# Kernel tuning notes

Measured on AMD Instinct MI355X. Metric: run time of the kernel, lower is better.

The kernel has to match this reference:

```python
import jax, jax.numpy as jnp
import numpy as np

DIM = 1024
HEADS = 16
HEAD_DIM = DIM // HEADS
K = 13              # kernel_size (odd)
NS = K // 2         # neighborhood radius
SCALE = HEAD_DIM ** -0.5


def setup_inputs() -> dict:
    key = jax.random.key(0)
    ks = jax.random.split(key, 5)
    B, L = 2, 4096
    x = jax.random.normal(ks[0], (B, L, DIM), jnp.float32)
    qkv_w = jax.random.normal(ks[1], (3 * DIM, DIM), jnp.float32) * 0.02
    qkv_b = jnp.zeros((3 * DIM,), jnp.float32)
    rpb = jax.random.normal(ks[2], (HEADS, 2 * K - 1), jnp.float32) * 0.02  # trunc_normal std=0.02
    proj_w = jax.random.normal(ks[3], (DIM, DIM), jnp.float32) * 0.02
    proj_b = jnp.zeros((DIM,), jnp.float32)
    return dict(x=x, qkv_w=qkv_w, qkv_b=qkv_b, rpb=rpb, proj_w=proj_w, proj_b=proj_b)


def reference(x, qkv_w, qkv_b, rpb, proj_w, proj_b):
    B, L, C = x.shape
    # qkv projection (torch Linear convention: y = x @ W^T + b)
    qkv = (x @ qkv_w.T + qkv_b).reshape(B, L, 3, HEADS, HEAD_DIM).transpose(2, 0, 3, 1, 4)
    q, k, v = qkv[0] * SCALE, qkv[1], qkv[2]  # each [B, H, L, D]

    i = jnp.arange(L)
    # NATTEN 1D window start (dilation=1): clamp window fully inside [0, L)
    ni = jnp.clip(i - NS, 0, L - K)                       # [L]
    # relative-position-bias start index per query (NATTEN get_pb_start)
    pi = NS + jnp.where(i < NS, NS - i, 0) + jnp.where(i + NS >= L, L - i - 1 - NS, 0)  # [L]
    j = jnp.arange(K)
    nbr = ni[:, None] + j[None, :]                        # [L, K] neighbor key indices
    bidx = pi[:, None] + j[None, :]                       # [L, K] rpb indices in [0, 2K-2]

    kg = k[:, :, nbr, :]                                  # [B, H, L, K, D]
    vg = v[:, :, nbr, :]                                  # [B, H, L, K, D]

    attn = jnp.einsum('bhld,bhlkd->bhlk', q, kg) + rpb[:, bidx][None]  # [B, H, L, K]
    attn = jax.nn.softmax(attn, axis=-1)
    out = jnp.einsum('bhlk,bhlkd->bhld', attn, vg)        # [B, H, L, D]
    out = out.transpose(0, 2, 1, 3).reshape(B, L, C)
    return out @ proj_w.T + proj_b
```

## Files before the change

kernel.cpp:

```cpp
#include <hip/hip_runtime.h>
#include <hip/hip_bf16.h>

#define DIMC 1024
#define HEADS 16
#define HEAD_DIM 64
#define KWIN 13
#define NSH 6
#define LSEQ 4096
#define BATCH 2
#define NROWS (BATCH*LSEQ)
#define QKV_N (3*DIMC)
#define SCALE_Q 0.125f

#define TBLK 256
#define WROWS 268

typedef __attribute__((ext_vector_type(4))) float f32x4;
typedef __attribute__((ext_vector_type(8))) short bf16x8;

__device__ __forceinline__ void gload_lds16(const void* g, void* l) {
  __builtin_amdgcn_global_load_lds(
      (const __attribute__((address_space(1))) void*)g,
      (__attribute__((address_space(3))) void*)l, 16, 0, 0);
}

__device__ __forceinline__ void cvt8(uint4 r, float* f) {
  unsigned u[4] = {r.x, r.y, r.z, r.w};
#pragma unroll
  for (int w = 0; w < 4; w++) {
    f[2*w]   = __uint_as_float(u[w] << 16);
    f[2*w+1] = __uint_as_float(u[w] & 0xffff0000u);
  }
}

__global__ __launch_bounds__(256) void cast_kernel(const float* __restrict__ in,
                                                   __hip_bfloat16* __restrict__ out,
                                                   int n4) {
  int i = blockIdx.x * 256 + threadIdx.x;
  if (i >= n4) return;
  float4 v = ((const float4*)in)[i];
  union { short4 s; __hip_bfloat16 h[4]; } u;
  u.h[0] = __float2bfloat16(v.x);
  u.h[1] = __float2bfloat16(v.y);
  u.h[2] = __float2bfloat16(v.z);
  u.h[3] = __float2bfloat16(v.w);
  ((short4*)out)[i] = u.s;
}

template<int OUT_BF16>
__global__ __launch_bounds__(256) void gemm_bt(const __hip_bfloat16* __restrict__ A,
                                               const __hip_bfloat16* __restrict__ B,
                                               const float* __restrict__ bias,
                                               void* __restrict__ Cout,
                                               int M, int N, int K) {
  __shared__ __align__(16) __hip_bfloat16 As[128 * 32];
  __shared__ __align__(16) __hip_bfloat16 Bs[128 * 32];

  const int tid  = threadIdx.x;
  const int lane = tid & 63;
  const int wave = tid >> 6;
  const int m0 = blockIdx.y * 128;
  const int n0 = blockIdx.x * 128;
  const int wr = wave >> 1;
  const int wc = wave & 1;

  f32x4 acc[4][4] = {};

  const int rA0  = wave * 32 + (lane >> 2);
  const int kcol = (lane & 3) * 8;
  const __hip_bfloat16* gA = A + (size_t)(m0 + rA0) * K + kcol;
  const __hip_bfloat16* gB = B + (size_t)(n0 + rA0) * K + kcol;
  __hip_bfloat16* lA0 = As + wave * 1024;
  __hip_bfloat16* lA1 = As + wave * 1024 + 512;
  __hip_bfloat16* lB0 = Bs + wave * 1024;
  __hip_bfloat16* lB1 = Bs + wave * 1024 + 512;

  const int fr = lane & 15;
  const int fk = (lane >> 4) * 8;

  for (int k0 = 0; k0 < K; k0 += 32) {
    gload_lds16(gA,                  lA0);
    gload_lds16(gA + (size_t)16 * K, lA1);
    gload_lds16(gB,                  lB0);
    gload_lds16(gB + (size_t)16 * K, lB1);
    gA += 32;
    gB += 32;
    __syncthreads();

    bf16x8 af[4], bfr[4];
#pragma unroll
    for (int i = 0; i < 4; i++)
      af[i] = *(const bf16x8*)&As[(wr * 64 + i * 16 + fr) * 32 + fk];
#pragma unroll
    for (int i = 0; i < 4; i++)
      bfr[i] = *(const bf16x8*)&Bs[(wc * 64 + i * 16 + fr) * 32 + fk];

#pragma unroll
    for (int mi = 0; mi < 4; mi++)
#pragma unroll
      for (int ni = 0; ni < 4; ni++)
        acc[mi][ni] = __builtin_amdgcn_mfma_f32_16x16x32_bf16(af[mi], bfr[ni], acc[mi][ni], 0, 0, 0);

    __syncthreads();
  }

#pragma unroll
  for (int ni = 0; ni < 4; ni++) {
    const int col = n0 + wc * 64 + ni * 16 + (lane & 15);
    const float bv = bias[col];
#pragma unroll
    for (int mi = 0; mi < 4; mi++) {
      const int row = m0 + wr * 64 + mi * 16 + ((lane >> 4) << 2);
#pragma unroll
      for (int i = 0; i < 4; i++) {
        const float v = acc[mi][ni][i] + bv;
        if (OUT_BF16)
          ((__hip_bfloat16*)Cout)[(size_t)(row + i) * N + col] = __float2bfloat16(v);
        else
          ((float*)Cout)[(size_t)(row + i) * N + col] = v;
      }
    }
  }
}

__global__ __launch_bounds__(256, 2) void natten(const __hip_bfloat16* __restrict__ qkv,
                                                 const float* __restrict__ rpb,
                                                 __hip_bfloat16* __restrict__ att) {
  __shared__ __align__(16) unsigned char smem[2 * WROWS * 128];

  const int tid = threadIdx.x;
  const int tb  = blockIdx.x;
  const int h   = blockIdx.y;
  const int b   = blockIdx.z;
  const int t0  = tb * TBLK;

  int r0 = t0 - NSH;
  if (r0 < 0) r0 = 0;
  if (r0 > LSEQ - WROWS) r0 = LSEQ - WROWS;

  const __hip_bfloat16* kg = qkv + ((size_t)b * LSEQ + r0) * QKV_N + DIMC + h * HEAD_DIM;
  const __hip_bfloat16* vg = kg + DIMC;
#pragma unroll 1
  for (int i = tid; i < WROWS * 8; i += 256) {
    const int row = i >> 3, c = i & 7;
    const uint4 kk = *(const uint4*)(kg + (size_t)row * QKV_N + c * 8);
    const uint4 vv = *(const uint4*)(vg + (size_t)row * QKV_N + c * 8);
    const int off = row * 128 + ((c * 16) ^ ((row & 7) << 4));
    *(uint4*)(smem + off) = kk;
    *(uint4*)(smem + WROWS * 128 + off) = vv;
  }
  __syncthreads();

  const int t = t0 + tid;
  int ni = t - NSH;
  ni = ni < 0 ? 0 : (ni > LSEQ - KWIN ? LSEQ - KWIN : ni);
  const int rbase = ni - r0;
  const int pi = NSH + (t < NSH ? NSH - t : 0) + (t + NSH >= LSEQ ? LSEQ - t - 1 - NSH : 0);
  const float* rp = rpb + h * (2 * KWIN - 1) + pi;

  const __hip_bfloat16* qg = qkv + ((size_t)b * LSEQ + t) * QKV_N + h * HEAD_DIM;
  float qf[64];
#pragma unroll
  for (int c = 0; c < 8; c++) {
    uint4 qq = *(const uint4*)(qg + c * 8);
    cvt8(qq, qf + c * 8);
  }

  float p[KWIN];
#pragma unroll
  for (int j = 0; j < KWIN; j++) {
    const int row = rbase + j;
    const int sw = (row & 7) << 4;
    float s = 0.f;
#pragma unroll
    for (int c = 0; c < 8; c++) {
      uint4 kk = *(const uint4*)(smem + row * 128 + ((c * 16) ^ sw));
      float kf[8];
      cvt8(kk, kf);
#pragma unroll
      for (int e = 0; e < 8; e++) s += qf[c * 8 + e] * kf[e];
    }
    p[j] = s * SCALE_Q + rp[j];
  }

  float m = p[0];
#pragma unroll
  for (int j = 1; j < KWIN; j++) m = fmaxf(m, p[j]);
  float sum = 0.f;
#pragma unroll
  for (int j = 0; j < KWIN; j++) { p[j] = __expf(p[j] - m); sum += p[j]; }
  const float inv = 1.f / sum;
#pragma unroll
  for (int j = 0; j < KWIN; j++) p[j] *= inv;

  __hip_bfloat16* og = att + ((size_t)b * LSEQ + t) * DIMC + h * HEAD_DIM;
#pragma unroll
  for (int c = 0; c < 8; c++) {
    float acc[8] = {0.f, 0.f, 0.f, 0.f, 0.f, 0.f, 0.f, 0.f};
#pragma unroll
    for (int j = 0; j < KWIN; j++) {
      const int row = rbase + j;
      uint4 vv = *(const uint4*)(smem + WROWS * 128 + row * 128 + ((c * 16) ^ ((row & 7) << 4)));
      float vf[8];
      cvt8(vv, vf);
#pragma unroll
      for (int e = 0; e < 8; e++) acc[e] += p[j] * vf[e];
    }
    union { ushort us[8]; uint4 v; } o;
#pragma unroll
    for (int e = 0; e < 8; e++) {
      __hip_bfloat16 hb = __float2bfloat16(acc[e]);
      o.us[e] = *(ushort*)&hb;
    }
    *(uint4*)(og + c * 8) = o.v;
  }
}

extern "C" void kernel_launch(void* const* d_in, const int* in_sizes, int n_in,
                              void* d_out, int out_size, void* d_ws, size_t ws_size,
                              hipStream_t stream) {
  const float* x      = (const float*)d_in[0];
  const float* qkv_w  = (const float*)d_in[1];
  const float* qkv_b  = (const float*)d_in[2];
  const float* rpb    = (const float*)d_in[3];
  const float* proj_w = (const float*)d_in[4];
  const float* proj_b = (const float*)d_in[5];
  float* out = (float*)d_out;

  char* ws = (char*)d_ws;
  __hip_bfloat16* xb    = (__hip_bfloat16*)(ws);
  __hip_bfloat16* wqkv  = (__hip_bfloat16*)(ws + 16777216);
  __hip_bfloat16* wproj = (__hip_bfloat16*)(ws + 23068672);
  __hip_bfloat16* qkv   = (__hip_bfloat16*)(ws + 25165824);
  __hip_bfloat16* att   = (__hip_bfloat16*)(ws + 75497472);

  cast_kernel<<<(NROWS * DIMC / 4 + 255) / 256, 256, 0, stream>>>(x, xb, NROWS * DIMC / 4);
  cast_kernel<<<(QKV_N * DIMC / 4 + 255) / 256, 256, 0, stream>>>(qkv_w, wqkv, QKV_N * DIMC / 4);
  cast_kernel<<<(DIMC * DIMC / 4 + 255) / 256, 256, 0, stream>>>(proj_w, wproj, DIMC * DIMC / 4);

  gemm_bt<1><<<dim3(QKV_N / 128, NROWS / 128), 256, 0, stream>>>(
      xb, wqkv, qkv_b, (void*)qkv, NROWS, QKV_N, DIMC);

  natten<<<dim3(LSEQ / TBLK, HEADS, BATCH), 256, 0, stream>>>(qkv, rpb, att);

  gemm_bt<0><<<dim3(DIMC / 128, NROWS / 128), 256, 0, stream>>>(
      att, wproj, proj_b, (void*)out, NROWS, DIMC, DIMC);
}
```

Baseline: 149.5 us.

## Replace QKV GEMM with 256x256 tiled, double-buffered 8-wave pipelined kernel

Adds a new bf16 GEMM for the QKV projection with 256x256 tiles, 8 waves, 64-wide K steps, and double-buffered LDS fed by direct global-to-LDS loads. Fine-grained vmcnt waits, barriers and s_setprio interleave the staging with MFMA phases. Block IDs are remapped across XCDs, and the epilogue goes through LDS to write 16-byte bf16 stores. It aims to raise MFMA utilization and hide load latency in the largest GEMM, at the cost of 128KB of LDS and hand-scheduled code that is harder to keep correct. The loop runs NT/2 iterations, which assumes an even tile count; that holds for K=1024.

Measured after the change: 203.3 us. 1.36x slower.

```diff
diff --git a/kernel.cpp b/kernel.cpp
--- a/kernel.cpp
+++ b/kernel.cpp
@@ -47,6 +47,146 @@
   ((short4*)out)[i] = u.s;
 }
 
+#define PH_MID do { __builtin_amdgcn_s_barrier(); \
+  asm volatile("s_waitcnt lgkmcnt(0)" ::: "memory"); \
+  __builtin_amdgcn_sched_barrier(0); \
+  __builtin_amdgcn_s_setprio(1); } while (0)
+#define PH_END do { __builtin_amdgcn_s_setprio(0); \
+  __builtin_amdgcn_s_barrier(); } while (0)
+#define VMW4 do { asm volatile("s_waitcnt vmcnt(4)" ::: "memory"); \
+  __builtin_amdgcn_sched_barrier(0); } while (0)
+
+#define STG(gptr, ldsoff) do { \
+  gload_lds16((const void*)(gptr),      (void*)(smem + (ldsoff) + w * 2048)); \
+  gload_lds16((const void*)((gptr)+q8), (void*)(smem + (ldsoff) + w * 2048 + 1024)); \
+} while (0)
+#define STAGE_A(buf, h, t) STG(((h) ? gA1 : gA0) + (size_t)(t) * 64, (buf)*32768 + (h)*16384)
+#define STAGE_B(buf, h, t) STG(((h) ? gB1 : gB0) + (size_t)(t) * 64, 65536 + (buf)*32768 + (h)*16384)
+
+#define LD_A4(buf, mb) do { _Pragma("unroll") for (int mm = 0; mm < 4; mm++) { \
+    const char* p_ = smem + (buf)*32768 + (rA + ((mb) + mm) * 16) * 128; \
+    afr[mm][0] = *(const bf16x8*)(p_ + ck0); \
+    afr[mm][1] = *(const bf16x8*)(p_ + ck1); } } while (0)
+#define LD_B2(buf, nb, dst) do { _Pragma("unroll") for (int nn = 0; nn < 2; nn++) { \
+    const char* p_ = smem + 65536 + (buf)*32768 + (rB + ((nb) + nn) * 16) * 128; \
+    dst[nn][0] = *(const bf16x8*)(p_ + ck0); \
+    dst[nn][1] = *(const bf16x8*)(p_ + ck1); } } while (0)
+#define MM16(mb, bsel, bf) do { _Pragma("unroll") for (int mm = 0; mm < 4; mm++) \
+  _Pragma("unroll") for (int nn = 0; nn < 2; nn++) { \
+    acc[(mb)+mm][(bsel)*2+nn] = __builtin_amdgcn_mfma_f32_16x16x32_bf16(afr[mm][0], bf[nn][0], acc[(mb)+mm][(bsel)*2+nn], 0, 0, 0); \
+    acc[(mb)+mm][(bsel)*2+nn] = __builtin_amdgcn_mfma_f32_16x16x32_bf16(afr[mm][1], bf[nn][1], acc[(mb)+mm][(bsel)*2+nn], 0, 0, 0); } } while (0)
+
+__global__ __launch_bounds__(512, 2) void gemm8(const __hip_bfloat16* __restrict__ A,
+                                                const __hip_bfloat16* __restrict__ B,
+                                                const float* __restrict__ bias,
+                                                __hip_bfloat16* __restrict__ C,
+                                                int M, int N, int K) {
+  __shared__ __align__(16) char smem[131072];
+  const int tid  = threadIdx.x;
+  const int lane = tid & 63;
+  const int w    = tid >> 6;
+  const int wm   = w >> 2;
+  const int wn   = w & 3;
+  const int fr   = lane & 15;
+  const int fq   = (lane >> 4) & 3;
+
+  int id = blockIdx.x;
+  {
+    const int nwg = gridDim.x;
+    const int qq = nwg >> 3, rr = nwg & 7;
+    const int xcd = id & 7, off = id >> 3;
+    id = (xcd < rr ? xcd * (qq + 1) : rr * (qq + 1) + (xcd - rr) * qq) + off;
+  }
+  const int nbx = N >> 8;
+  const int bx = id % nbx, by = id / nbx;
+  const int m0 = by << 8, n0 = bx << 8;
+
+  const int srow = w * 16 + (lane >> 3);
+  const int gch  = ((lane & 7) ^ (lane >> 3)) * 8;
+  const __hip_bfloat16* gA0 = A + (size_t)(m0 + srow) * K + gch;
+  const __hip_bfloat16* gA1 = A + (size_t)(m0 + 128 + srow) * K + gch;
+  const __hip_bfloat16* gB0 = B + (size_t)(n0 + srow) * K + gch;
+  const __hip_bfloat16* gB1 = B + (size_t)(n0 + 128 + srow) * K + gch;
+  const size_t q8 = (size_t)8 * K;
+
+  const int rA  = wm * 128 + fr;
+  const int rB  = wn * 64 + fr;
+  const int ck0 = ((fq)     ^ (fr & 7)) * 16;
+  const int ck1 = ((4 | fq) ^ (fr & 7)) * 16;
+
+  f32x4 acc[8][4] = {};
+  bf16x8 afr[4][2], bfr0[2][2], bfr1[2][2];
+
+  STAGE_A(0, 0, 0); STAGE_A(0, 1, 0);
+  STAGE_B(0, 0, 0); STAGE_B(0, 1, 0);
+  STAGE_B(1, 0, 1); STAGE_B(1, 1, 1);
+  VMW4;
+  __builtin_amdgcn_s_barrier();
+
+  const int NT = K >> 6;
+  const int NI = NT >> 1;
+#pragma unroll 1
+  for (int i = 0; i < NI; i++) {
+    const int t1 = (2*i+1 < NT) ? 2*i+1 : NT-1;
+    const int t2 = (2*i+2 < NT) ? 2*i+2 : NT-1;
+    const int t3 = (2*i+3 < NT) ? 2*i+3 : NT-1;
+    LD_A4(0, 0); LD_B2(0, 0, bfr0);
+    STAGE_A(1, 0, t1);
+    PH_MID; MM16(0, 0, bfr0); PH_END;
+    LD_B2(0, 2, bfr1);
+    STAGE_A(1, 1, t1);
+    PH_MID; MM16(0, 1, bfr1); PH_END;
+    LD_A4(0, 4);
+    STAGE_B(0, 0, t2);
+    PH_MID; MM16(4, 0, bfr0); PH_END;
+    STAGE_B(0, 1, t2);
+    VMW4;
+    PH_MID; MM16(4, 1, bfr1); PH_END;
+    LD_A4(1, 0); LD_B2(1, 0, bfr0);
+    STAGE_A(0, 0, t2);
+    PH_MID; MM16(0, 0, bfr0); PH_END;
+    LD_B2(1, 2, bfr1);
+    STAGE_A(0, 1, t2);
+    PH_MID; MM16(0, 1, bfr1); PH_END;
+    LD_A4(1, 4);
+    STAGE_B(1, 0, t3);
+    PH_MID; MM16(4, 0, bfr0); PH_END;
+    STAGE_B(1, 1, t3);
+    VMW4;
+    PH_MID; MM16(4, 1, bfr1); PH_END;
+  }
+
+  asm volatile("s_waitcnt vmcnt(0)" ::: "memory");
+  __builtin_amdgcn_sched_barrier(0);
+  __builtin_amdgcn_s_barrier();
+
+  float* sf = (float*)(smem) + w * 1088;
+  float bv[4];
+#pragma unroll
+  for (int n = 0; n < 4; n++) bv[n] = bias[n0 + wn * 64 + n * 16 + fr];
+
+#pragma unroll 1
+  for (int m = 0; m < 8; m++) {
+#pragma unroll
+    for (int n = 0; n < 4; n++)
+#pragma unroll
+      for (int i = 0; i < 4; i++)
+        sf[(fq * 4 + i) * 68 + n * 16 + fr] = acc[m][n][i] + bv[n];
+    float v[16];
+#pragma unroll
+    for (int e = 0; e < 16; e++) v[e] = sf[fr * 68 + fq * 16 + e];
+    union { ushort us[16]; uint4 u4[2]; } o;
+#pragma unroll
+    for (int e = 0; e < 16; e++) {
+      __hip_bfloat16 hb = __float2bfloat16(v[e]);
+      o.us[e] = *(ushort*)&hb;
+    }
+    __hip_bfloat16* cp = C + (size_t)(m0 + wm * 128 + m * 16 + fr) * N + n0 + wn * 64 + fq * 16;
+    *(uint4*)(cp)     = o.u4[0];
+    *(uint4*)(cp + 8) = o.u4[1];
+  }
+}
+
 template<int OUT_BF16>
 __global__ __launch_bounds__(256) void gemm_bt(const __hip_bfloat16* __restrict__ A,
                                                const __hip_bfloat16* __restrict__ B,
@@ -238,8 +378,8 @@
   cast_kernel<<<(QKV_N * DIMC / 4 + 255) / 256, 256, 0, stream>>>(qkv_w, wqkv, QKV_N * DIMC / 4);
   cast_kernel<<<(DIMC * DIMC / 4 + 255) / 256, 256, 0, stream>>>(proj_w, wproj, DIMC * DIMC / 4);
 
-  gemm_bt<1><<<dim3(QKV_N / 128, NROWS / 128), 256, 0, stream>>>(
-      xb, wqkv, qkv_b, (void*)qkv, NROWS, QKV_N, DIMC);
+  gemm8<<<(NROWS / 256) * (QKV_N / 256), 512, 0, stream>>>(
+      xb, wqkv, qkv_b, qkv, NROWS, QKV_N, DIMC);
 
   natten<<<dim3(LSEQ / TBLK, HEADS, BATCH), 256, 0, stream>>>(qkv, rpb, att);
 
```
